# Performance work log

Hardware: AMD Instinct MI355X
Metric: run time of the kernel (lower is better)

Reference implementation:

```python
import jax, jax.numpy as jnp
import numpy as np

B, L, C, Y, DIM = 64, 64, 4, 0, 2  # batch, lattice size, n_colors, tau-shift, shift axis


def _coloring_probes():
    # k x k block coloring for C colors (C must be a perfect square here; C=4 -> k=2)
    k = int(round(np.sqrt(C)))
    i = np.arange(L)[:, None]
    j = np.arange(L)[None, :]
    col = (i % k) * k + (j % k)  # (L, L) color index per site
    probes = (col[None, :, :] == np.arange(C)[:, None, None]).astype(np.float32)
    return jnp.asarray(probes)  # (C, L, L) one-hot color masks


def _gelu(x):
    return jax.nn.gelu(x, approximate=False)  # torch nn.GELU default = exact erf


def _forward(x, sW1, sb1, sW2, sb2, sW3, sb3, aW1, ab1, aW2, ab2):
    # site features: phi, 2D lattice laplacian (periodic), phi_{x+tau}, phi_{x-tau}
    lap = (jnp.roll(x, 1, 1) + jnp.roll(x, -1, 1)
           + jnp.roll(x, 1, 2) + jnp.roll(x, -1, 2) - 4.0 * x)
    phi_tau = jnp.roll(x, -Y, axis=DIM)
    phi_mtau = jnp.roll(x, Y, axis=DIM)
    f = jnp.stack([x, lap, phi_tau, phi_mtau], axis=-1)  # (B, L, L, 4)
    h = _gelu(f @ sW1 + sb1)
    h = _gelu(h @ sW2 + sb2)
    h = (h @ sW3 + sb3)[..., 0]                          # (B, L, L)
    h_mean = h.mean(axis=(1, 2))
    h_var = jnp.var(h, axis=(1, 2), ddof=1)              # torch .var() is unbiased
    h_sq_mean = (h * h).mean(axis=(1, 2))
    a = jnp.stack([h_mean, h_var, h_sq_mean], axis=1)    # (B, 3)
    a = _gelu(a @ aW1 + ab1)
    return (a @ aW2 + ab2)[..., 0]                       # (B,)


def setup_inputs() -> dict:
    key = jax.random.key(0)
    ks = jax.random.split(key, 8)

    def w(k, shape, fan_in):
        return jax.random.normal(k, shape, jnp.float32) / np.sqrt(fan_in).astype(np.float32)

    return {
        "x": jax.random.normal(ks[0], (B, L, L), jnp.float32),
        "signs": jax.random.randint(ks[1], (C, B, L, L), 0, 2, jnp.int32),
        "site_W1": w(ks[2], (4, 128), 4),
        "site_b1": jnp.zeros((128,), jnp.float32),
        "site_W2": w(ks[3], (128, 128), 128),
        "site_b2": jnp.zeros((128,), jnp.float32),
        "site_W3": w(ks[4], (128, 1), 128),
        "site_b3": jnp.zeros((1,), jnp.float32),
        "agg_W1": w(ks[5], (3, 64), 3),
        "agg_b1": jnp.zeros((64,), jnp.float32),
        "agg_W2": w(ks[6], (64, 1), 64),
        "agg_b2": jnp.zeros((1,), jnp.float32),
    }


def reference(x, signs, site_W1, site_b1, site_W2, site_b2, site_W3, site_b3,
              agg_W1, agg_b1, agg_W2, agg_b2):
    params = (site_W1, site_b1, site_W2, site_b2, site_W3, site_b3,
              agg_W1, agg_b1, agg_W2, agg_b2)
    fsum = lambda xx: _forward(xx, *params).sum()  # batches are independent, so sum is safe

    # first-order gradient grad_x F, shape (B, L, L)
    grad = jax.grad(fsum)(x)

    # probing laplacian with coloring + Rademacher signs, batched over colors
    probes = _coloring_probes()                                   # (C, L, L)
    z = (2.0 * signs.astype(jnp.float32) - 1.0) * probes[:, None]  # (C, B, L, L)
    # hvp_c = H @ z_c via forward-over-reverse AD (replaces per-color autograd.grad loop)
    hvp = jax.vmap(lambda zc: jax.jvp(jax.grad(fsum), (x,), (zc,))[1])(z)  # (C, B, L, L)
    lapl = jnp.sum(hvp * z, axis=(0, 2, 3))                       # (B,)

    # pack (grad, lapl) into one array: (B, L*L + 1)
    return jnp.concatenate([grad.reshape(B, -1), lapl[:, None]], axis=1)
```

## Files before the change

### kernel.cpp

```cpp
#include <hip/hip_runtime.h>
#include <hip/hip_bf16.h>
#include <math.h>

typedef unsigned short ushort_t;
typedef unsigned int   u32;
typedef __attribute__((ext_vector_type(8))) short s8v;
typedef __attribute__((ext_vector_type(4))) float f4v;
typedef __attribute__((ext_vector_type(2))) float f2v;

#define LL 64
#define NB 64
#define NSITE 4096
#define BN 262144
#define RED_OFF 0
#define LP_OFF  10240
#define WA_OFF  11264
#define WB_OFF  11392
#define PL_OFF  12288
#define BF_OFF  (PL_OFF + 6*BN)

#if __has_builtin(__builtin_amdgcn_exp2f)
#define EXP2F(x) __builtin_amdgcn_exp2f(x)
#else
#define EXP2F(x) __expf(0.6931471805599453f*(x))
#endif

__device__ __forceinline__ void gelu3(float u, float &h, float &d, float &e){
  float E   = __expf(-0.5f * u * u);
  float phi = 0.3989422804014327f * E;
  float az  = fabsf(u) * 0.70710678118654752f;
  float t   = __builtin_amdgcn_rcpf(1.0f + 0.3275911f * az);
  float p   = t*(0.254829592f + t*(-0.284496736f + t*(1.421413741f + t*(-1.453152027f + t*1.061405429f))));
  float erfabs = 1.0f - p * E;
  float erfv   = __builtin_copysignf(erfabs, u);
  float Phi = 0.5f * (1.0f + erfv);
  h = u * Phi;
  d = Phi + u * phi;
  e = phi * (2.0f - u * u);
}

__device__ __forceinline__ void gelu3x2(f2v u, f2v &h, f2v &d, f2v &e){
  f2v u2 = u * u;
  f2v m  = u2 * (-0.72134752044448170368f);
  f2v E;  E.x = EXP2F(m.x); E.y = EXP2F(m.y);
  f2v phi = 0.3989422804014327f * E;
  f2v az;
  az.x = fabsf(u.x) * 0.70710678118654752f;
  az.y = fabsf(u.y) * 0.70710678118654752f;
  f2v den = 0.3275911f * az + 1.0f;
  f2v t;  t.x = __builtin_amdgcn_rcpf(den.x); t.y = __builtin_amdgcn_rcpf(den.y);
  f2v p = t*(0.254829592f + t*(-0.284496736f + t*(1.421413741f + t*(-1.453152027f + t*1.061405429f))));
  f2v erfabs = 1.0f - p * E;
  f2v erfv;
  erfv.x = __builtin_copysignf(erfabs.x, u.x);
  erfv.y = __builtin_copysignf(erfabs.y, u.y);
  f2v Phi = 0.5f * erfv + 0.5f;
  h = u * Phi;
  d = u * phi + Phi;
  e = phi * (2.0f - u2);
}

#define DPP_ADD(v, ctrl) { \
  int _si = __builtin_amdgcn_update_dpp(0, __builtin_bit_cast(int, v), ctrl, 0xf, 0xf, true); \
  v += __builtin_bit_cast(float, _si); }

__device__ __forceinline__ float redjb16(float v){
  DPP_ADD(v, 0xB1);
  DPP_ADD(v, 0x4E);
  DPP_ADD(v, 0x124);
  DPP_ADD(v, 0x128);
  return v;
}
__device__ __forceinline__ float red64(float v){
  v = redjb16(v);
  v += __shfl_xor(v, 16);
  v += __shfl_xor(v, 32);
  return v;
}

__device__ __forceinline__ float redpair(float a, float b, bool hi8){
  float t = hi8 ? b : a;
  float o = hi8 ? a : b;
  int _s = __builtin_amdgcn_update_dpp(0, __builtin_bit_cast(int, o), 0x128, 0xf, 0xf, true);
  t += __builtin_bit_cast(float, _s);
  DPP_ADD(t, 0xB1);
  DPP_ADD(t, 0x4E);
  DPP_ADD(t, 0x141);
  return t;
}

__device__ __forceinline__ ushort_t bf16rne(float v){
  union { float f; u32 i; } x; x.f = v;
  u32 r = x.i + 0x7FFFu + ((x.i >> 16) & 1u);
  return (ushort_t)(r >> 16);
}
__device__ __forceinline__ u32 pkbf(float a, float b){
  __hip_bfloat162 t = __float22bfloat162_rn(make_float2(a, b));
  u32 r;
  __builtin_memcpy(&r, &t, sizeof(r));
  return r;
}
__device__ __forceinline__ u32 pkbf2(f2v v){
  return pkbf(v.x, v.y);
}

__global__ __launch_bounds__(256, 4) void k_pre(
    const float* __restrict__ W1g, const float* __restrict__ W2g,
    float* __restrict__ ws)
{
  int t = blockIdx.x * 256 + threadIdx.x;
  if (blockIdx.x == 0 && threadIdx.x < 128) {
    int k = threadIdx.x;
    ws[WA_OFF + k] = W1g[k] + W1g[256+k] + W1g[384+k];
    ws[WB_OFF + k] = W1g[128+k];
  }
  short* BF = (short*)(ws + BF_OFF);
  int w = t >> 9, nt = (t >> 8) & 1, kt = (t >> 6) & 3, lane = t & 63;
  int q = lane >> 4, nlo = lane & 15;
  int n = w*32 + nt*16 + nlo;
  s8v vh;
  #pragma unroll
  for (int jj = 0; jj < 8; ++jj) {
    int k = kt*32 + q*8 + jj;
    vh[jj] = (short)bf16rne(W2g[k*128 + n]);
  }
  *(s8v*)&BF[t*8] = vh;
}

__global__ __launch_bounds__(256, 4) void k_c1(
    const float* __restrict__ xg, const int* __restrict__ signs,
    const float* __restrict__ b1g, const float* __restrict__ b2g,
    const float* __restrict__ W3g, const float* __restrict__ b3g,
    float* __restrict__ ws)
{
  __shared__ alignas(16) short AF[12288];
  __shared__ float xS[6][64];
  __shared__ char  zS[6][64];
  __shared__ float EP[16][7][4];

  const int tid  = threadIdx.x;
  const int lane = tid & 63;
  const int w    = tid >> 6;
  const int q    = lane >> 4;
  const int nlo  = lane & 15;
  const bool hi8 = (nlo & 8) != 0;

  const int blk = blockIdx.x;
  const int b   = blk >> 4;
  const int i0  = (blk & 15) << 2;

  const s8v* BhT = (const s8v*)((const short*)(ws + BF_OFF)) + (w*512 + lane);

  float b2j[2], w3j[2];
  #pragma unroll
  for (int nt = 0; nt < 2; ++nt) {
    int j = w*32 + nt*16 + nlo;
    b2j[nt] = b2g[j];
    w3j[nt] = W3g[j];
  }
  float b3v = b3g[0];
  const f2v b2p = {b2j[0], b2j[1]};
  const f2v w3p = {w3j[0], w3j[1]};

  const int s_  = tid & 15;
  const int ko_ = tid >> 4;
  float4 waH[2], wbH[2], b1H[2];
  #pragma unroll
  for (int half = 0; half < 2; ++half) {
    int k0 = ko_*8 + half*4;
    waH[half] = *(const float4*)(ws + WA_OFF + k0);
    wbH[half] = *(const float4*)(ws + WB_OFF + k0);
    b1H[half] = *(const float4*)(b1g + k0);
  }

  for (int t = tid; t < 384; t += 256) {
    int r = t >> 6, j = t & 63;
    int gr = (i0 - 1 + r) & 63;
    xS[r][j] = xg[(size_t)b*NSITE + gr*64 + j];
    int c = ((gr & 1) << 1) | (j & 1);
    zS[r][j] = (char)(2*signs[((c*NB + b)*LL + gr)*LL + j] - 1);
  }
  __syncthreads();

  float racc[10];
  #pragma unroll
  for (int n = 0; n < 10; ++n) racc[n] = 0.f;

  #pragma unroll 1
  for (int ch = 0; ch < 16; ++ch) {
    const int lr = 1 + (ch >> 2);
    const int jb = ch & 3;
    const int i  = i0 + (ch >> 2);

    {
      int j = jb*16 + s_, jm = (j+63)&63, jp = (j+1)&63;
      float p = xS[lr][j];
      float l = xS[lr-1][j] + xS[lr+1][j] + xS[lr][jm] + xS[lr][jp] - 4.0f*p;
      u32 vv[6][4];
      #pragma unroll
      for (int half = 0; half < 2; ++half) {
        const float* waA = (const float*)&waH[half];
        const float* wbA = (const float*)&wbH[half];
        const float* b1A = (const float*)&b1H[half];
        #pragma unroll
        for (int pr = 0; pr < 2; ++pr) {
          f2v wa = {waA[pr*2], waA[pr*2+1]};
          f2v wb = {wbA[pr*2], wbA[pr*2+1]};
          f2v bb = {b1A[pr*2], b1A[pr*2+1]};
          f2v u = p*wa + l*wb + bb;
          f2v h, dd, ee;
          gelu3x2(u, h, dd, ee);
          int c = half*2 + pr;
          vv[0][c] = pkbf2(h);
          vv[1][c] = pkbf2(dd*wa);
          vv[2][c] = pkbf2(dd*wb);
          f2v ea = ee*wa, eb = ee*wb;
          vv[3][c] = pkbf2(ea*wa);
          vv[4][c] = pkbf2(ea*wb);
          vv[5][c] = pkbf2(eb*wb);
        }
      }
      short* base = &AF[(ko_>>2)*3072 + ((ko_&3)*16 + s_)*8];
      #pragma unroll
      for (int pp = 0; pp < 6; ++pp)
        *(int4*)&base[pp*512] = make_int4((int)vv[pp][0], (int)vv[pp][1],
                                          (int)vv[pp][2], (int)vv[pp][3]);
    }
    __syncthreads();

    f4v acc[6][2];
    #pragma unroll
    for (int pp = 0; pp < 6; ++pp)
      #pragma unroll
      for (int nt = 0; nt < 2; ++nt)
        acc[pp][nt] = (f4v){0.f, 0.f, 0.f, 0.f};

    s8v bh0 = BhT[0], bh1 = BhT[256];
    #pragma unroll 1
    for (int kt = 0; kt < 4; ++kt) {
      s8v nh0 = bh0, nh1 = bh1;
      if (kt != 3) {
        int o = (kt + 1) * 64;
        nh0 = BhT[o]; nh1 = BhT[256 + o];
      }
      const short* base = &AF[kt*3072 + lane*8];
      #pragma unroll
      for (int pp = 0; pp < 6; ++pp) {
        s8v ah = *(const s8v*)&base[pp*512];
        acc[pp][0] = __builtin_amdgcn_mfma_f32_16x16x32_bf16(ah, bh0, acc[pp][0], 0, 0, 0);
        acc[pp][1] = __builtin_amdgcn_mfma_f32_16x16x32_bf16(ah, bh1, acc[pp][1], 0, 0, 0);
      }
      bh0 = nh0; bh1 = nh1;
    }

    {
      #pragma unroll
      for (int r = 0; r < 4; ++r) {
        f2v uu = (f2v){acc[0][0][r], acc[0][1][r]} + b2p;
        f2v h2, d2, e2;
        gelu3x2(uu, h2, d2, e2);
        f2v wd = w3p*d2, we = w3p*e2;
        f2v A  = (f2v){acc[1][0][r], acc[1][1][r]};
        f2v Bv = (f2v){acc[2][0][r], acc[2][1][r]};
        f2v t3 = (f2v){acc[3][0][r], acc[3][1][r]};
        f2v t4 = (f2v){acc[4][0][r], acc[4][1][r]};
        f2v t5 = (f2v){acc[5][0][r], acc[5][1][r]};
        f2v vsh = w3p*h2;
        f2v vsA = wd*A;
        f2v vsB = wd*Bv;
        f2v vsa = we*(A*A)   + wd*t3;
        f2v vsb = we*(A*Bv)  + wd*t4;
        f2v vsc = we*(Bv*Bv) + wd*t5;
        float sh = vsh.x + vsh.y;
        float sA = vsA.x + vsA.y;
        float sB = vsB.x + vsB.y;
        float sa = vsa.x + vsa.y;
        float sb = vsb.x + vsb.y;
        float sc = vsc.x + vsc.y;
        float r01 = redpair(sh, sA, hi8);
        float r23 = redpair(sB, sa, hi8);
        float r45 = redpair(sb, sc, hi8);
        if ((nlo & 7) == 0) {
          int site = q*4 + r;
          int off = nlo >> 3;
          EP[site][0+off][w] = r01;
          EP[site][2+off][w] = r23;
          EP[site][4+off][w] = r45;
        }
      }
    }
    __syncthreads();

    if (tid < 16) {
      int s = tid;
      float h = 0.f, RA = 0.f, RB = 0.f, TAa = 0.f, TAb = 0.f, TBb = 0.f;
      #pragma unroll
      for (int ww = 0; ww < 4; ++ww) {
        h   += EP[s][0][ww];
        RA  += EP[s][1][ww];
        RB  += EP[s][2][ww];
        TAa += EP[s][3][ww];
        TAb += EP[s][4][ww];
        TBb += EP[s][5][ww];
      }
      h += b3v;
      float* P = ws + PL_OFF;
      int j = jb*16 + s;
      size_t site = (size_t)b*NSITE + i*64 + j;
      P[0*BN + site] = h;
      P[1*BN + site] = RA;
      P[2*BN + site] = RB;
      P[3*BN + site] = TAa;
      P[4*BN + site] = TAb;
      P[5*BN + site] = TBb;

      int jm = (j+63)&63, jp = (j+1)&63;
      int c0 = ((i & 1) << 1) | (j & 1);
      float hd[4] = {0.f, 0.f, 0.f, 0.f};
      hd[c0]     = (float)zS[lr][j] * (RA - 4.0f*RB);
      hd[c0 ^ 1] = (float)(zS[lr][jm] + zS[lr][jp]) * RB;
      hd[c0 ^ 2] = (float)(zS[lr-1][j] + zS[lr+1][j]) * RB;
      racc[0] += h;
      racc[1] += h*h;
      #pragma unroll
      for (int cc = 0; cc < 4; ++cc) {
        racc[2+cc] += hd[cc];
        racc[6+cc] += h*hd[cc];
      }
    }
  }

  if (tid < 16) {
    #pragma unroll
    for (int n = 0; n < 10; ++n) racc[n] = redjb16(racc[n]);
    if (tid == 0) {
      #pragma unroll
      for (int n = 0; n < 10; ++n) ws[RED_OFF + blk*10 + n] = racc[n];
    }
  }
}

__global__ __launch_bounds__(256, 1) void k_c2(
    const int* __restrict__ signs,
    const float* __restrict__ aW1g, const float* __restrict__ ab1g,
    const float* __restrict__ aW2g,
    float* __restrict__ ws, float* __restrict__ out)
{
  __shared__ float part[4];
  __shared__ float coefL[10];
  __shared__ float redS[10];
  __shared__ float cbS[6][64];
  int blk = blockIdx.x;
  int b = blk >> 4, rg = blk & 15;
  int tid = threadIdx.x;

  if (tid < 160) {
    int qq = tid >> 4, g = tid & 15;
    float v = ws[RED_OFF + (b*16 + g)*10 + qq];
    v = redjb16(v);
    if (g == 0) redS[qq] = v;
  }
  __syncthreads();

  if (tid < 64) {
    int k = tid;
    const float Nf = 4096.0f, Nm1 = 4095.0f;
    float S1 = redS[0], S2 = redS[1];
    float m = S1/Nf, q = S2/Nf;
    float v = (S2 - S1*S1/Nf)/Nm1;
    float w0 = aW1g[k], w1 = aW1g[64+k], w2 = aW1g[128+k];
    float t = m*w0 + v*w1 + q*w2 + ab1g[k];
    float gh, gd, ge;
    gelu3(t, gh, gd, ge);
    float o = aW2g[k];
    float g1o = gd*o, g2o = ge*o;
    float da0 = w0*g1o, da1 = w1*g1o, da2 = w2*g1o;
    float M00 = w0*w0*g2o, M01 = w0*w1*g2o, M02 = w0*w2*g2o;
    float M11 = w1*w1*g2o, M12 = w1*w2*g2o, M22 = w2*w2*g2o;
    da0 = red64(da0); da1 = red64(da1); da2 = red64(da2);
    M00 = red64(M00); M01 = red64(M01); M02 = red64(M02);
    M11 = red64(M11); M12 = red64(M12); M22 = red64(M22);
    if (k == 0) {
      coefL[0] = da0/Nf - 2.0f*da1*m/Nm1;
      coefL[1] = 2.0f*da1/Nm1 + 2.0f*da2/Nf;
      #pragma unroll
      for (int c = 0; c < 4; ++c) {
        float s1 = redS[2 + c], s2 = redS[6 + c];
        float md = s1/Nf, qd = 2.0f*s2/Nf;
        float vd = (2.0f*s2 - 2.0f*S1*s1/Nf)/Nm1;
        float dd0 = M00*md + M01*vd + M02*qd;
        float dd1 = M01*md + M11*vd + M12*qd;
        float dd2 = M02*md + M12*vd + M22*qd;
        coefL[2+c] = dd0/Nf - 2.0f*(dd1*m + da1*md)/Nm1;
        coefL[6+c] = 2.0f*dd1/Nm1 + 2.0f*dd2/Nf;
      }
    }
  }
  __syncthreads();

  const float* P = ws + PL_OFF;
  int base = b*NSITE;
  float alpha = coefL[0], beta = coefL[1];

  for (int t = tid; t < 384; t += 256) {
    int r = t >> 6, jj = t & 63;
    int gr = (rg*4 - 1 + r) & 63;
    int sidx = base + gr*64 + jj;
    cbS[r][jj] = (alpha + beta*P[sidx]) * P[2*BN + sidx];
  }
  __syncthreads();

  int rl = tid >> 6, j = tid & 63;
  int i = rg*4 + rl;
  int im=(i+63)&63, ip=(i+1)&63, jm=(j+63)&63, jp=(j+1)&63;
  int s  = base + i*64 + j;
  float h  = P[s], RA = P[BN+s], RB = P[2*BN+s];
  float TAa= P[3*BN+s], TAb = P[4*BN+s], TBb = P[5*BN+s];
  float g  = alpha + beta*h;
  int lr2 = rl + 1;
  float cb  = cbS[lr2][j];
  float cbu = cbS[lr2-1][j], cbd = cbS[lr2+1][j];
  float cbl = cbS[lr2][jm],  cbr = cbS[lr2][jp];
  float grad = g*RA + (cbu + cbd + cbl + cbr - 4.0f*cb);
  out[(size_t)b*4097 + i*64 + j] = grad;

  int c0 = ((i & 1) << 1) | (j & 1);
  int c1 = c0 ^ 1, c2 = c0 ^ 2;
  float zv = 2.0f*(float)signs[((c0*NB + b)*LL + i )*LL + j ] - 1.0f;
  float zl = 2.0f*(float)signs[((c1*NB + b)*LL + i )*LL + jm] - 1.0f;
  float zr = 2.0f*(float)signs[((c1*NB + b)*LL + i )*LL + jp] - 1.0f;
  float zu = 2.0f*(float)signs[((c2*NB + b)*LL + im)*LL + j ] - 1.0f;
  float zd = 2.0f*(float)signs[((c2*NB + b)*LL + ip)*LL + j ] - 1.0f;
  float sjr = zl + zr, sud = zu + zd;
  float hd0 = zv*(RA - 4.0f*RB);
  float hd1 = sjr*RB, hd2 = sud*RB;
  float gd0 = coefL[2+c0] + coefL[6+c0]*h + beta*hd0;
  float gd1 = coefL[2+c1] + coefL[6+c1]*h + beta*hd1;
  float gd2 = coefL[2+c2] + coefL[6+c2]*h + beta*hd2;
  float ca0 = gd0*RA + g*( zv*TAa - 4.0f*zv*TAb );
  float cb0 = gd0*RB + g*( zv*TAb - 4.0f*zv*TBb );
  float cb1 = gd1*RB + g*( sjr*TBb );
  float cb2 = gd2*RB + g*( sud*TBb );
  float contrib = zv*ca0 - 4.0f*zv*cb0 + sjr*cb1 + sud*cb2;

  float vsum = red64(contrib);
  int wv = tid >> 6;
  if ((tid & 63) == 0) part[wv] = vsum;
  __syncthreads();
  if (tid == 0)
    ws[LP_OFF + blk] = part[0] + part[1] + part[2] + part[3];
}

__global__ void k_e(const float* __restrict__ ws, float* __restrict__ out){
  int b = threadIdx.x;
  if (b < 64) {
    float s = 0.f;
    #pragma unroll
    for (int g = 0; g < 16; ++g) s += ws[LP_OFF + b*16 + g];
    out[(size_t)b*4097 + 4096] = s;
  }
}

extern "C" void kernel_launch(void* const* d_in, const int* in_sizes, int n_in,
                              void* d_out, int out_size, void* d_ws, size_t ws_size,
                              hipStream_t stream) {
  const float* xg    = (const float*)d_in[0];
  const int*   signs = (const int*)d_in[1];
  const float* W1    = (const float*)d_in[2];
  const float* b1    = (const float*)d_in[3];
  const float* W2    = (const float*)d_in[4];
  const float* b2    = (const float*)d_in[5];
  const float* W3    = (const float*)d_in[6];
  const float* b3    = (const float*)d_in[7];
  const float* aW1   = (const float*)d_in[8];
  const float* ab1   = (const float*)d_in[9];
  const float* aW2   = (const float*)d_in[10];
  float* ws  = (float*)d_ws;
  float* out = (float*)d_out;

  hipLaunchKernelGGL(k_pre, dim3(8),    dim3(256), 0, stream, W1, W2, ws);
  hipLaunchKernelGGL(k_c1,  dim3(1024), dim3(256), 0, stream,
                     xg, signs, b1, b2, W3, b3, ws);
  hipLaunchKernelGGL(k_c2,  dim3(1024), dim3(256), 0, stream,
                     signs, aW1, ab1, aW2, ws, out);
  hipLaunchKernelGGL(k_e,   dim3(1),    dim3(64),  0, stream, ws, out);
}
```

Baseline: 196.1 us.

## Swap MFMA operands to cut epilogue reductions and drop final reduce kernel

The MFMA operand order is swapped so each lane's accumulator holds four hidden units of one site. The epilogue can then sum over units in registers and needs only two cross-row shuffles instead of DPP pair reductions. The first k-step is peeled to feed zero accumulators directly, and s_setprio is raised around the MFMA loop. The final reduction kernel is replaced by atomicAdd into the output, which k_pre now zeroes. This removes one launch but makes the float summation order nondeterministic.

```diff
diff --git a/kernel.cpp b/kernel.cpp
--- a/kernel.cpp
+++ b/kernel.cpp
@@ -78,17 +78,6 @@
   return v;
 }
 
-__device__ __forceinline__ float redpair(float a, float b, bool hi8){
-  float t = hi8 ? b : a;
-  float o = hi8 ? a : b;
-  int _s = __builtin_amdgcn_update_dpp(0, __builtin_bit_cast(int, o), 0x128, 0xf, 0xf, true);
-  t += __builtin_bit_cast(float, _s);
-  DPP_ADD(t, 0xB1);
-  DPP_ADD(t, 0x4E);
-  DPP_ADD(t, 0x141);
-  return t;
-}
-
 __device__ __forceinline__ ushort_t bf16rne(float v){
   union { float f; u32 i; } x; x.f = v;
   u32 r = x.i + 0x7FFFu + ((x.i >> 16) & 1u);
@@ -106,13 +95,16 @@
 
 __global__ __launch_bounds__(256, 4) void k_pre(
     const float* __restrict__ W1g, const float* __restrict__ W2g,
-    float* __restrict__ ws)
+    float* __restrict__ ws, float* __restrict__ out)
 {
   int t = blockIdx.x * 256 + threadIdx.x;
   if (blockIdx.x == 0 && threadIdx.x < 128) {
     int k = threadIdx.x;
     ws[WA_OFF + k] = W1g[k] + W1g[256+k] + W1g[384+k];
     ws[WB_OFF + k] = W1g[128+k];
+  }
+  if (blockIdx.x == 1 && threadIdx.x < 64) {
+    out[(size_t)threadIdx.x*4097 + 4096] = 0.f;
   }
   short* BF = (short*)(ws + BF_OFF);
   int w = t >> 9, nt = (t >> 8) & 1, kt = (t >> 6) & 3, lane = t & 63;
@@ -141,9 +133,7 @@
   const int tid  = threadIdx.x;
   const int lane = tid & 63;
   const int w    = tid >> 6;
-  const int q    = lane >> 4;
-  const int nlo  = lane & 15;
-  const bool hi8 = (nlo & 8) != 0;
+  const int rg4  = (lane >> 4) << 2;
 
   const int blk = blockIdx.x;
   const int b   = blk >> 4;
@@ -151,16 +141,14 @@
 
   const s8v* BhT = (const s8v*)((const short*)(ws + BF_OFF)) + (w*512 + lane);
 
-  float b2j[2], w3j[2];
+  float4 b2H[2], w3H[2];
   #pragma unroll
   for (int nt = 0; nt < 2; ++nt) {
-    int j = w*32 + nt*16 + nlo;
-    b2j[nt] = b2g[j];
-    w3j[nt] = W3g[j];
+    int n0 = w*32 + nt*16 + rg4;
+    b2H[nt] = *(const float4*)(b2g + n0);
+    w3H[nt] = *(const float4*)(W3g + n0);
   }
   float b3v = b3g[0];
-  const f2v b2p = {b2j[0], b2j[1]};
-  const f2v w3p = {w3j[0], w3j[1]};
 
   const int s_  = tid & 15;
   const int ko_ = tid >> 4;
@@ -185,6 +173,8 @@
   float racc[10];
   #pragma unroll
   for (int n = 0; n < 10; ++n) racc[n] = 0.f;
+
+  const f4v Zf = {0.f, 0.f, 0.f, 0.f};
 
   #pragma unroll 1
   for (int ch = 0; ch < 16; ++ch) {
@@ -229,15 +219,21 @@
     __syncthreads();
 
     f4v acc[6][2];
-    #pragma unroll
-    for (int pp = 0; pp < 6; ++pp)
-      #pragma unroll
-      for (int nt = 0; nt < 2; ++nt)
-        acc[pp][nt] = (f4v){0.f, 0.f, 0.f, 0.f};
-
+    __builtin_amdgcn_s_setprio(1);
     s8v bh0 = BhT[0], bh1 = BhT[256];
+    {
+      s8v nh0 = BhT[64], nh1 = BhT[320];
+      const short* base = &AF[lane*8];
+      #pragma unroll
+      for (int pp = 0; pp < 6; ++pp) {
+        s8v ah = *(const s8v*)&base[pp*512];
+        acc[pp][0] = __builtin_amdgcn_mfma_f32_16x16x32_bf16(bh0, ah, Zf, 0, 0, 0);
+        acc[pp][1] = __builtin_amdgcn_mfma_f32_16x16x32_bf16(bh1, ah, Zf, 0, 0, 0);
+      }
+      bh0 = nh0; bh1 = nh1;
+    }
     #pragma unroll 1
-    for (int kt = 0; kt < 4; ++kt) {
+    for (int kt = 1; kt < 4; ++kt) {
       s8v nh0 = bh0, nh1 = bh1;
       if (kt != 3) {
         int o = (kt + 1) * 64;
@@ -247,46 +243,61 @@
       #pragma unroll
       for (int pp = 0; pp < 6; ++pp) {
         s8v ah = *(const s8v*)&base[pp*512];
-        acc[pp][0] = __builtin_amdgcn_mfma_f32_16x16x32_bf16(ah, bh0, acc[pp][0], 0, 0, 0);
-        acc[pp][1] = __builtin_amdgcn_mfma_f32_16x16x32_bf16(ah, bh1, acc[pp][1], 0, 0, 0);
+        acc[pp][0] = __builtin_amdgcn_mfma_f32_16x16x32_bf16(bh0, ah, acc[pp][0], 0, 0, 0);
+        acc[pp][1] = __builtin_amdgcn_mfma_f32_16x16x32_bf16(bh1, ah, acc[pp][1], 0, 0, 0);
       }
       bh0 = nh0; bh1 = nh1;
     }
+    __builtin_amdgcn_s_setprio(0);
 
     {
-      #pragma unroll
-      for (int r = 0; r < 4; ++r) {
-        f2v uu = (f2v){acc[0][0][r], acc[0][1][r]} + b2p;
-        f2v h2, d2, e2;
-        gelu3x2(uu, h2, d2, e2);
-        f2v wd = w3p*d2, we = w3p*e2;
-        f2v A  = (f2v){acc[1][0][r], acc[1][1][r]};
-        f2v Bv = (f2v){acc[2][0][r], acc[2][1][r]};
-        f2v t3 = (f2v){acc[3][0][r], acc[3][1][r]};
-        f2v t4 = (f2v){acc[4][0][r], acc[4][1][r]};
-        f2v t5 = (f2v){acc[5][0][r], acc[5][1][r]};
-        f2v vsh = w3p*h2;
-        f2v vsA = wd*A;
-        f2v vsB = wd*Bv;
-        f2v vsa = we*(A*A)   + wd*t3;
-        f2v vsb = we*(A*Bv)  + wd*t4;
-        f2v vsc = we*(Bv*Bv) + wd*t5;
-        float sh = vsh.x + vsh.y;
-        float sA = vsA.x + vsA.y;
-        float sB = vsB.x + vsB.y;
-        float sa = vsa.x + vsa.y;
-        float sb = vsb.x + vsb.y;
-        float sc = vsc.x + vsc.y;
-        float r01 = redpair(sh, sA, hi8);
-        float r23 = redpair(sB, sa, hi8);
-        float r45 = redpair(sb, sc, hi8);
-        if ((nlo & 7) == 0) {
-          int site = q*4 + r;
-          int off = nlo >> 3;
-          EP[site][0+off][w] = r01;
-          EP[site][2+off][w] = r23;
-          EP[site][4+off][w] = r45;
+      f2v qh = {0.f,0.f}, qA = {0.f,0.f}, qB = {0.f,0.f};
+      f2v qa = {0.f,0.f}, qb = {0.f,0.f}, qc = {0.f,0.f};
+      #pragma unroll
+      for (int nt = 0; nt < 2; ++nt) {
+        const float* b2A = (const float*)&b2H[nt];
+        const float* w3A = (const float*)&w3H[nt];
+        #pragma unroll
+        for (int pr = 0; pr < 2; ++pr) {
+          const int r0 = pr*2;
+          f2v uu  = (f2v){acc[0][nt][r0], acc[0][nt][r0+1]}
+                  + (f2v){b2A[r0], b2A[r0+1]};
+          f2v w3p = {w3A[r0], w3A[r0+1]};
+          f2v h2, d2, e2;
+          gelu3x2(uu, h2, d2, e2);
+          f2v wd = w3p*d2, we = w3p*e2;
+          f2v A  = {acc[1][nt][r0], acc[1][nt][r0+1]};
+          f2v Bv = {acc[2][nt][r0], acc[2][nt][r0+1]};
+          f2v t3 = {acc[3][nt][r0], acc[3][nt][r0+1]};
+          f2v t4 = {acc[4][nt][r0], acc[4][nt][r0+1]};
+          f2v t5 = {acc[5][nt][r0], acc[5][nt][r0+1]};
+          qh += w3p*h2;
+          qA += wd*A;
+          qB += wd*Bv;
+          qa += we*(A*A)   + wd*t3;
+          qb += we*(A*Bv)  + wd*t4;
+          qc += we*(Bv*Bv) + wd*t5;
         }
+      }
+      float sh = qh.x + qh.y;
+      float sA = qA.x + qA.y;
+      float sB = qB.x + qB.y;
+      float sa = qa.x + qa.y;
+      float sb = qb.x + qb.y;
+      float sc = qc.x + qc.y;
+      sh += __shfl_xor(sh, 16); sh += __shfl_xor(sh, 32);
+      sA += __shfl_xor(sA, 16); sA += __shfl_xor(sA, 32);
+      sB += __shfl_xor(sB, 16); sB += __shfl_xor(sB, 32);
+      sa += __shfl_xor(sa, 16); sa += __shfl_xor(sa, 32);
+      sb += __shfl_xor(sb, 16); sb += __shfl_xor(sb, 32);
+      sc += __shfl_xor(sc, 16); sc += __shfl_xor(sc, 32);
+      if (lane < 16) {
+        EP[lane][0][w] = sh;
+        EP[lane][1][w] = sA;
+        EP[lane][2][w] = sB;
+        EP[lane][3][w] = sa;
+        EP[lane][4][w] = sb;
+        EP[lane][5][w] = sc;
       }
     }
     __syncthreads();
@@ -448,17 +459,8 @@
   if ((tid & 63) == 0) part[wv] = vsum;
   __syncthreads();
   if (tid == 0)
-    ws[LP_OFF + blk] = part[0] + part[1] + part[2] + part[3];
-}
-
-__global__ void k_e(const float* __restrict__ ws, float* __restrict__ out){
-  int b = threadIdx.x;
-  if (b < 64) {
-    float s = 0.f;
-    #pragma unroll
-    for (int g = 0; g < 16; ++g) s += ws[LP_OFF + b*16 + g];
-    out[(size_t)b*4097 + 4096] = s;
-  }
+    atomicAdd(out + (size_t)b*4097 + 4096,
+              part[0] + part[1] + part[2] + part[3]);
 }
 
 extern "C" void kernel_launch(void* const* d_in, const int* in_sizes, int n_in,
@@ -478,10 +480,9 @@
   float* ws  = (float*)d_ws;
   float* out = (float*)d_out;
 
-  hipLaunchKernelGGL(k_pre, dim3(8),    dim3(256), 0, stream, W1, W2, ws);
+  hipLaunchKernelGGL(k_pre, dim3(8),    dim3(256), 0, stream, W1, W2, ws, out);
   hipLaunchKernelGGL(k_c1,  dim3(1024), dim3(256), 0, stream,
                      xg, signs, b1, b2, W3, b3, ws);
   hipLaunchKernelGGL(k_c2,  dim3(1024), dim3(256), 0, stream,
                      signs, aW1, ab1, aW2, ws, out);
-  hipLaunchKernelGGL(k_e,   dim3(1),    dim3(64),  0, stream, ws, out);
-}
+}
```

Result: faster. 190.7 us (-2.8%).
